# Performance work log

Hardware: AMD Instinct MI355X
Metric: run time of the kernel (lower is better)

Reference implementation:

```python
import jax, jax.numpy as jnp
import numpy as np
import math

D_MODEL = 1024
N_HEADS = 16
B, L, K = 2, 512, 4


def sinusoidal_pe(n, dim):
    # matches SinusoidalEmbedding buffer pe[:n]
    position = jnp.arange(n, dtype=jnp.float32)[:, None]
    div_term = jnp.exp(jnp.arange(0, dim, 2, dtype=jnp.float32) * (-math.log(10000.0) / dim))
    ang = position * div_term  # [n, dim//2]
    pe = jnp.zeros((n, dim), dtype=jnp.float32)
    pe = pe.at[:, 0::2].set(jnp.sin(ang))
    pe = pe.at[:, 1::2].set(jnp.cos(ang))
    return pe


def setup_inputs() -> dict:
    key = jax.random.key(0)
    ks = jax.random.split(key, 8)
    s = 1.0 / math.sqrt(D_MODEL)
    return {
        "h": jax.random.normal(ks[0], (B, L, K, D_MODEL), dtype=jnp.float32),
        "probs": jax.random.uniform(ks[1], (B, L, K), dtype=jnp.float32),
        "Wq": jax.random.normal(ks[2], (D_MODEL, D_MODEL), dtype=jnp.float32) * s,
        "bq": jnp.zeros((D_MODEL,), dtype=jnp.float32),
        "Wk": jax.random.normal(ks[3], (D_MODEL, D_MODEL), dtype=jnp.float32) * s,
        "bk": jnp.zeros((D_MODEL,), dtype=jnp.float32),
        "Wv": jax.random.normal(ks[4], (D_MODEL, D_MODEL), dtype=jnp.float32) * s,
        "bv": jnp.zeros((D_MODEL,), dtype=jnp.float32),
        "Wo": jax.random.normal(ks[5], (D_MODEL, D_MODEL), dtype=jnp.float32) * s,
        "bo": jnp.zeros((D_MODEL,), dtype=jnp.float32),
        "prob_bias_scale": jnp.float32(1.0),
        "n_heads": N_HEADS,
    }


def reference(h, probs, Wq, bq, Wk, bk, Wv, bv, Wo, bo, prob_bias_scale, n_heads):
    Bh, Lh, kh, D = h.shape
    N = Lh * kh
    hd = D // n_heads
    scale = hd ** (-0.5)

    h_flat = h.reshape(Bh, N, D) + sinusoidal_pe(N, D)[None]  # [B, N, D]
    probs_flat = probs.reshape(Bh, N)

    # torch Linear: x @ W.T + b
    q = (h_flat @ Wq.T + bq).reshape(Bh, N, n_heads, hd).transpose(0, 2, 1, 3)
    key = (h_flat @ Wk.T + bk).reshape(Bh, N, n_heads, hd).transpose(0, 2, 1, 3)
    v = (h_flat @ Wv.T + bv).reshape(Bh, N, n_heads, hd).transpose(0, 2, 1, 3)

    scores = jnp.einsum("bhnd,bhmd->bhnm", q, key) * scale  # [B,H,N,N]
    prob_bias = jnp.log(probs_flat + 1e-8)[:, None, None, :]  # bias on key axis
    scores = scores + prob_bias_scale * prob_bias
    attn = jax.nn.softmax(scores, axis=-1)  # dropout is identity in eval
    out = jnp.einsum("bhnm,bhmd->bhnd", attn, v)
    out = out.transpose(0, 2, 1, 3).reshape(Bh, N, D)
    out = out @ Wo.T + bo
    return out.reshape(Bh, Lh, kh, D)
```

## Files before the change

kernel.cpp:

```cpp
#include <hip/hip_runtime.h>

typedef _Float16 h8 __attribute__((ext_vector_type(8)));
typedef _Float16 h4 __attribute__((ext_vector_type(4)));
typedef float f32x4 __attribute__((ext_vector_type(4)));

#define NSEQ 2048
#define DMODEL 1024
#define HD 64
#define C2 0.1803368801111244f

#define OFF_HPE  (size_t)0
#define OFF_WQ   (size_t)8388608
#define OFF_WK   (size_t)10485760
#define OFF_WV   (size_t)12582912
#define OFF_WO   (size_t)14680064
#define OFF_Q    (size_t)16777216
#define OFF_K    (size_t)25165824
#define OFF_VT   (size_t)33554432
#define OFF_AO   (size_t)41943040
#define OFF_PB   (size_t)50331648

#define GLL(g, l) __builtin_amdgcn_global_load_lds( \
    (const __attribute__((address_space(1))) unsigned int*)(const void*)(g), \
    (__attribute__((address_space(3))) unsigned int*)(l), 16, 0, 0)

#if __has_builtin(__builtin_amdgcn_mfma_f32_16x16x16f16)
#define HAVE_MFMA16 1
#else
#define HAVE_MFMA16 0
#endif

__global__ void hpe_kernel(const float* __restrict__ h, _Float16* __restrict__ hpe) {
    int idx = blockIdx.x * blockDim.x + threadIdx.x;
    int row = idx >> 9;
    int i2  = idx & 511;
    int n = row & (NSEQ - 1);
    const float kTerm = -9.210340371976184f / 1024.0f;
    float div = expf((float)(2 * i2) * kTerm);
    float ang = (float)n * div;
    float s = sinf(ang), c = cosf(ang);
    int base = row * DMODEL + 2 * i2;
    hpe[base]     = (_Float16)(h[base] + s);
    hpe[base + 1] = (_Float16)(h[base + 1] + c);
}

__global__ void cast4_kernel(const float* __restrict__ w0, const float* __restrict__ w1,
                             const float* __restrict__ w2, const float* __restrict__ w3,
                             _Float16* __restrict__ d0, _Float16* __restrict__ d1,
                             _Float16* __restrict__ d2, _Float16* __restrict__ d3) {
    int i = blockIdx.x * blockDim.x + threadIdx.x;
    int which = i >> 18, idx = i & 262143;
    const float* s = which == 0 ? w0 : which == 1 ? w1 : which == 2 ? w2 : w3;
    _Float16* d    = which == 0 ? d0 : which == 1 ? d1 : which == 2 ? d2 : d3;
    float4 v = ((const float4*)s)[idx];
    union { _Float16 hh[4]; uint2 u; } o;
    o.hh[0] = (_Float16)v.x; o.hh[1] = (_Float16)v.y;
    o.hh[2] = (_Float16)v.z; o.hh[3] = (_Float16)v.w;
    ((uint2*)d)[idx] = o.u;
}

__global__ void pb_kernel(const float* __restrict__ probs, const float* __restrict__ pbs,
                          float* __restrict__ pb) {
    int i = blockIdx.x * blockDim.x + threadIdx.x;
    pb[i] = pbs[0] * log2f(probs[i] + 1e-8f);
}

__global__ __launch_bounds__(256) void gemm_qkv(
    const _Float16* __restrict__ A,
    const _Float16* __restrict__ Wqp, const _Float16* __restrict__ Wkp, const _Float16* __restrict__ Wvp,
    const float* __restrict__ bqp, const float* __restrict__ bkp, const float* __restrict__ bvp,
    _Float16* __restrict__ qb, _Float16* __restrict__ kb, _Float16* __restrict__ vt)
{
    __shared__ __align__(16) _Float16 As[128][64];
    __shared__ __align__(16) _Float16 Bs[128][64];
    int widx = blockIdx.y >> 3;
    const _Float16* W = widx == 0 ? Wqp : widx == 1 ? Wkp : Wvp;
    const float* bias = widx == 0 ? bqp : widx == 1 ? bkp : bvp;
    int tm = blockIdx.x * 128;
    int tn = (blockIdx.y & 7) * 128;
    int t = threadIdx.x;
    int wave = t >> 6, lane = t & 63;
    int wr = (wave >> 1) * 64, wc = (wave & 1) * 64;
    int lr = lane & 15, lg = lane >> 4;

    f32x4 acc[4][4] = {};

    int grow = lane >> 3;
    int gcol = (lane & 7) * 8;
    const _Float16* Aptr = A + (size_t)(tm + wave * 8 + grow) * DMODEL + gcol;
    const _Float16* Wptr = W + (size_t)(tn + wave * 8 + grow) * DMODEL + gcol;

    for (int k0 = 0; k0 < DMODEL; k0 += 64) {
        __syncthreads();
        #pragma unroll
        for (int i = 0; i < 4; ++i)
            GLL(Aptr + (size_t)i * 32 * DMODEL + k0, &As[i * 32 + wave * 8][0]);
        #pragma unroll
        for (int i = 0; i < 4; ++i)
            GLL(Wptr + (size_t)i * 32 * DMODEL + k0, &Bs[i * 32 + wave * 8][0]);
        __syncthreads();
        #pragma unroll
        for (int kk = 0; kk < 2; ++kk) {
            h8 af[4], bf[4];
            #pragma unroll
            for (int mi = 0; mi < 4; ++mi) af[mi] = *(const h8*)&As[wr + mi * 16 + lr][kk * 32 + lg * 8];
            #pragma unroll
            for (int ni = 0; ni < 4; ++ni) bf[ni] = *(const h8*)&Bs[wc + ni * 16 + lr][kk * 32 + lg * 8];
            #pragma unroll
            for (int mi = 0; mi < 4; ++mi)
                #pragma unroll
                for (int ni = 0; ni < 4; ++ni)
                    acc[mi][ni] = __builtin_amdgcn_mfma_f32_16x16x32_f16(af[mi], bf[ni], acc[mi][ni], 0, 0, 0);
        }
    }

    #pragma unroll
    for (int mi = 0; mi < 4; ++mi)
        #pragma unroll
        for (int ni = 0; ni < 4; ++ni) {
            int col = tn + wc + ni * 16 + lr;
            float bv = bias[col];
            if (widx < 2) {
                _Float16* dst = widx == 0 ? qb : kb;
                #pragma unroll
                for (int j = 0; j < 4; ++j) {
                    int row = tm + wr + mi * 16 + lg * 4 + j;
                    dst[(size_t)row * DMODEL + col] = (_Float16)(acc[mi][ni][j] + bv);
                }
            } else {
                int row0 = tm + wr + mi * 16 + lg * 4;
                int b = row0 >> 11, n0 = row0 & 2047;
                h4 pk;
                #pragma unroll
                for (int j = 0; j < 4; ++j) pk[j] = (_Float16)(acc[mi][ni][j] + bv);
                *(h4*)&vt[((size_t)b * 1024 + col) * 2048 + n0] = pk;
            }
        }
}

__global__ __launch_bounds__(256) void gemm_ao(
    const _Float16* __restrict__ A, const _Float16* __restrict__ W,
    const float* __restrict__ bias, float* __restrict__ C)
{
    __shared__ __align__(16) _Float16 As[64][64];
    __shared__ __align__(16) _Float16 Bs[128][64];
    int tm = blockIdx.x * 64;
    int tn = blockIdx.y * 128;
    int t = threadIdx.x;
    int wave = t >> 6, lane = t & 63;
    int wr = (wave >> 1) * 32, wc = (wave & 1) * 64;
    int lr = lane & 15, lg = lane >> 4;

    f32x4 acc[2][4] = {};

    int grow = lane >> 3;
    int gcol = (lane & 7) * 8;
    const _Float16* Aptr = A + (size_t)(tm + wave * 8 + grow) * DMODEL + gcol;
    const _Float16* Wptr = W + (size_t)(tn + wave * 8 + grow) * DMODEL + gcol;

    for (int k0 = 0; k0 < DMODEL; k0 += 64) {
        __syncthreads();
        #pragma unroll
        for (int i = 0; i < 2; ++i)
            GLL(Aptr + (size_t)i * 32 * DMODEL + k0, &As[i * 32 + wave * 8][0]);
        #pragma unroll
        for (int i = 0; i < 4; ++i)
            GLL(Wptr + (size_t)i * 32 * DMODEL + k0, &Bs[i * 32 + wave * 8][0]);
        __syncthreads();
        #pragma unroll
        for (int kk = 0; kk < 2; ++kk) {
            h8 af[2], bf[4];
            #pragma unroll
            for (int mi = 0; mi < 2; ++mi) af[mi] = *(const h8*)&As[wr + mi * 16 + lr][kk * 32 + lg * 8];
            #pragma unroll
            for (int ni = 0; ni < 4; ++ni) bf[ni] = *(const h8*)&Bs[wc + ni * 16 + lr][kk * 32 + lg * 8];
            #pragma unroll
            for (int mi = 0; mi < 2; ++mi)
                #pragma unroll
                for (int ni = 0; ni < 4; ++ni)
                    acc[mi][ni] = __builtin_amdgcn_mfma_f32_16x16x32_f16(af[mi], bf[ni], acc[mi][ni], 0, 0, 0);
        }
    }

    #pragma unroll
    for (int mi = 0; mi < 2; ++mi)
        #pragma unroll
        for (int ni = 0; ni < 4; ++ni)
            #pragma unroll
            for (int j = 0; j < 4; ++j) {
                int row = tm + wr + mi * 16 + lg * 4 + j;
                int col = tn + wc + ni * 16 + lr;
                C[(size_t)row * DMODEL + col] = acc[mi][ni][j] + bias[col];
            }
}

#define QT 64
#define KT 64

#define SWZ(row, bytecol) ((row) * 128 + ((bytecol) ^ (((row) & 7) << 4)))

__global__ __launch_bounds__(256, 4) void flash_kernel(
    const _Float16* __restrict__ Qb,
    const _Float16* __restrict__ Kb,
    const _Float16* __restrict__ Vt,
    const float* __restrict__ pb,
    _Float16* __restrict__ AO)
{
    __shared__ __align__(16) char KsB[64 * 128];
    __shared__ __align__(16) char VsB[64 * 128];
#if !HAVE_MFMA16
    __shared__ __align__(16) _Float16 Ps[4][16][72];
#endif
    int bh = blockIdx.y;
    int b = bh >> 4, h = bh & 15;
    int q0 = blockIdx.x * QT;
    int t = threadIdx.x, wave = t >> 6, lane = t & 63;
    int lr = lane & 15, lg = lane >> 4;

    const _Float16* Khead  = Kb + (size_t)b * NSEQ * DMODEL + h * HD;
    const _Float16* Vthead = Vt + ((size_t)b * 1024 + h * HD) * NSEQ;
    const float* pbb = pb + b * NSEQ;

    const _Float16* Qrow = Qb + ((size_t)b * NSEQ + q0 + wave * 16 + lr) * DMODEL + h * HD;
    h8 qf0 = *(const h8*)&Qrow[lg * 8];
    h8 qf1 = *(const h8*)&Qrow[32 + lg * 8];

    float mrun = -INFINITY, lrun = 0.f;
    f32x4 oacc[4] = {};

    int srow = t >> 2;
    int sc = (t & 3) * 32;

    for (int k0 = 0; k0 < NSEQ; k0 += KT) {
        f32x4 pbv[4];
        #pragma unroll
        for (int ci = 0; ci < 4; ++ci)
            pbv[ci] = *(const f32x4*)&pbb[k0 + ci * 16 + lg * 4];

        __syncthreads();
        *(h8*)(KsB + SWZ(srow, sc))      = *(const h8*)&Khead[(size_t)(k0 + srow) * DMODEL + (sc >> 1)];
        *(h8*)(KsB + SWZ(srow, sc + 16)) = *(const h8*)&Khead[(size_t)(k0 + srow) * DMODEL + (sc >> 1) + 8];
        *(h8*)(VsB + SWZ(srow, sc))      = *(const h8*)&Vthead[(size_t)srow * NSEQ + k0 + (sc >> 1)];
        *(h8*)(VsB + SWZ(srow, sc + 16)) = *(const h8*)&Vthead[(size_t)srow * NSEQ + k0 + (sc >> 1) + 8];
        __syncthreads();

        f32x4 s[4] = {};
        #pragma unroll
        for (int ci = 0; ci < 4; ++ci) {
            h8 kf = *(const h8*)(KsB + SWZ(ci * 16 + lr, lg * 16));
            s[ci] = __builtin_amdgcn_mfma_f32_16x16x32_f16(kf, qf0, s[ci], 0, 0, 0);
        }
        #pragma unroll
        for (int ci = 0; ci < 4; ++ci) {
            h8 kf = *(const h8*)(KsB + SWZ(ci * 16 + lr, 64 + lg * 16));
            s[ci] = __builtin_amdgcn_mfma_f32_16x16x32_f16(kf, qf1, s[ci], 0, 0, 0);
        }

        float p[4][4];
        float sm = -INFINITY;
        #pragma unroll
        for (int ci = 0; ci < 4; ++ci)
            #pragma unroll
            for (int j = 0; j < 4; ++j) {
                float vv = fmaf(s[ci][j], C2, pbv[ci][j]);
                p[ci][j] = vv;
                sm = fmaxf(sm, vv);
            }
        sm = fmaxf(sm, __shfl_xor(sm, 16));
        sm = fmaxf(sm, __shfl_xor(sm, 32));
        float newm = fmaxf(mrun, sm);
        float fs = __builtin_amdgcn_exp2f(mrun - newm);
        float rs = 0.f;
        #pragma unroll
        for (int ci = 0; ci < 4; ++ci)
            #pragma unroll
            for (int j = 0; j < 4; ++j) {
                float e = __builtin_amdgcn_exp2f(p[ci][j] - newm);
                p[ci][j] = e;
                rs += e;
            }
        rs += __shfl_xor(rs, 16);
        rs += __shfl_xor(rs, 32);
        lrun = lrun * fs + rs;
        mrun = newm;

        #pragma unroll
        for (int j = 0; j < 4; ++j) {
            float fsj = __shfl(fs, (lane & 48) | (lg * 4 + j), 64);
            #pragma unroll
            for (int ni = 0; ni < 4; ++ni) oacc[ni][j] *= fsj;
        }

#if HAVE_MFMA16
        #pragma unroll
        for (int ci = 0; ci < 4; ++ci) {
            h4 pa;
            #pragma unroll
            for (int j = 0; j < 4; ++j) pa[j] = (_Float16)p[ci][j];
            #pragma unroll
            for (int ni = 0; ni < 4; ++ni) {
                h4 vf = *(const h4*)(VsB + SWZ(ni * 16 + lr, ci * 32 + lg * 8));
                oacc[ni] = __builtin_amdgcn_mfma_f32_16x16x16f16(pa, vf, oacc[ni], 0, 0, 0);
            }
        }
#else
        #pragma unroll
        for (int ci = 0; ci < 4; ++ci) {
            union { _Float16 hh[4]; uint2 u; } pk;
            #pragma unroll
            for (int j = 0; j < 4; ++j) pk.hh[j] = (_Float16)p[ci][j];
            *(uint2*)&Ps[wave][lr][ci * 16 + lg * 4] = pk.u;
        }
        asm volatile("s_waitcnt lgkmcnt(0)" ::: "memory");
        __builtin_amdgcn_sched_barrier(0);
        #pragma unroll
        for (int kb2 = 0; kb2 < 2; ++kb2) {
            h8 pa = *(const h8*)&Ps[wave][lr][kb2 * 32 + lg * 8];
            #pragma unroll
            for (int ni = 0; ni < 4; ++ni) {
                h8 vf = *(const h8*)(VsB + SWZ(ni * 16 + lr, kb2 * 64 + lg * 16));
                oacc[ni] = __builtin_amdgcn_mfma_f32_16x16x32_f16(pa, vf, oacc[ni], 0, 0, 0);
            }
        }
#endif
    }

    #pragma unroll
    for (int j = 0; j < 4; ++j) {
        float lj = __shfl(lrun, (lane & 48) | (lg * 4 + j), 64);
        float inv = 1.0f / lj;
        int row = q0 + wave * 16 + lg * 4 + j;
        #pragma unroll
        for (int ni = 0; ni < 4; ++ni)
            AO[((size_t)b * NSEQ + row) * DMODEL + h * HD + ni * 16 + lr] = (_Float16)(oacc[ni][j] * inv);
    }
}

extern "C" void kernel_launch(void* const* d_in, const int* in_sizes, int n_in,
                              void* d_out, int out_size, void* d_ws, size_t ws_size,
                              hipStream_t stream) {
    const float* h    = (const float*)d_in[0];
    const float* prob = (const float*)d_in[1];
    const float* Wq   = (const float*)d_in[2];
    const float* bq   = (const float*)d_in[3];
    const float* Wk   = (const float*)d_in[4];
    const float* bk   = (const float*)d_in[5];
    const float* Wv   = (const float*)d_in[6];
    const float* bv   = (const float*)d_in[7];
    const float* Wo   = (const float*)d_in[8];
    const float* bo   = (const float*)d_in[9];
    const float* pbs  = (const float*)d_in[10];

    char* ws = (char*)d_ws;
    _Float16* hpe  = (_Float16*)(ws + OFF_HPE);
    _Float16* wq16 = (_Float16*)(ws + OFF_WQ);
    _Float16* wk16 = (_Float16*)(ws + OFF_WK);
    _Float16* wv16 = (_Float16*)(ws + OFF_WV);
    _Float16* wo16 = (_Float16*)(ws + OFF_WO);
    _Float16* qb   = (_Float16*)(ws + OFF_Q);
    _Float16* kb16 = (_Float16*)(ws + OFF_K);
    _Float16* vt   = (_Float16*)(ws + OFF_VT);
    _Float16* ao   = (_Float16*)(ws + OFF_AO);
    float*    pbuf = (float*)(ws + OFF_PB);

    hpe_kernel<<<dim3(8192), dim3(256), 0, stream>>>(h, hpe);
    cast4_kernel<<<dim3(4096), dim3(256), 0, stream>>>(Wq, Wk, Wv, Wo, wq16, wk16, wv16, wo16);
    pb_kernel<<<dim3(16), dim3(256), 0, stream>>>(prob, pbs, pbuf);

    gemm_qkv<<<dim3(32, 24), dim3(256), 0, stream>>>(hpe, wq16, wk16, wv16, bq, bk, bv, qb, kb16, vt);

    flash_kernel<<<dim3(32, 32), dim3(256), 0, stream>>>(qb, kb16, vt, pbuf, ao);

    gemm_ao<<<dim3(64, 8), dim3(256), 0, stream>>>(ao, wo16, bo, (float*)d_out);
}
```

Measured before the change: 247.1 us.

## Fold softmax scale into Wq, lazy rescale, MFMA row sums, vectorize PE kernel

The softmax scale (log2e/sqrt(hd)) is folded into the Q weight cast and bias, so scores come straight out of the QK MFMA with the log-prob bias preloaded as the accumulator. The online softmax now rescales only when some row max increases (wave-wide vote), computes row sums with an extra MFMA against a ones vector, and always uses the LDS P path with V fragments loaded early. The positional-encoding kernel is vectorized to 8 elements per thread using hardware exp2/sin/cos on fractional revolutions. These changes cut per-tile VALU and shuffle work in attention and memory traffic in the prologue. In exchange there are extra MFMAs and some precision risk from the rtz packing and hardware trig.

```diff
diff --git a/kernel.cpp b/kernel.cpp
--- a/kernel.cpp
+++ b/kernel.cpp
@@ -2,6 +2,7 @@
 
 typedef _Float16 h8 __attribute__((ext_vector_type(8)));
 typedef _Float16 h4 __attribute__((ext_vector_type(4)));
+typedef __fp16 fp16x2 __attribute__((ext_vector_type(2)));
 typedef float f32x4 __attribute__((ext_vector_type(4)));
 
 #define NSEQ 2048
@@ -24,24 +25,29 @@
     (const __attribute__((address_space(1))) unsigned int*)(const void*)(g), \
     (__attribute__((address_space(3))) unsigned int*)(l), 16, 0, 0)
 
-#if __has_builtin(__builtin_amdgcn_mfma_f32_16x16x16f16)
-#define HAVE_MFMA16 1
-#else
-#define HAVE_MFMA16 0
-#endif
-
 __global__ void hpe_kernel(const float* __restrict__ h, _Float16* __restrict__ hpe) {
     int idx = blockIdx.x * blockDim.x + threadIdx.x;
-    int row = idx >> 9;
-    int i2  = idx & 511;
+    int row = idx >> 7;
+    int c8 = (idx & 127) * 8;
     int n = row & (NSEQ - 1);
-    const float kTerm = -9.210340371976184f / 1024.0f;
-    float div = expf((float)(2 * i2) * kTerm);
-    float ang = (float)n * div;
-    float s = sinf(ang), c = cosf(ang);
-    int base = row * DMODEL + 2 * i2;
-    hpe[base]     = (_Float16)(h[base] + s);
-    hpe[base + 1] = (_Float16)(h[base + 1] + c);
+    const float kL = -0.025952563241307517f;
+    const float kInv2Pi = 0.15915494309189535f;
+    union { float4 f4[2]; float f[8]; } in;
+    in.f4[0] = *(const float4*)&h[(size_t)row * DMODEL + c8];
+    in.f4[1] = *(const float4*)&h[(size_t)row * DMODEL + c8 + 4];
+    union { _Float16 hh[8]; uint4 u; } out;
+    #pragma unroll
+    for (int p = 0; p < 4; ++p) {
+        int i2 = (c8 >> 1) + p;
+        float div = __builtin_amdgcn_exp2f((float)i2 * kL);
+        float rev = (float)n * div * kInv2Pi;
+        float rf = __builtin_amdgcn_fractf(rev);
+        float s = __builtin_amdgcn_sinf(rf);
+        float c = __builtin_amdgcn_cosf(rf);
+        out.hh[2 * p]     = (_Float16)(in.f[2 * p] + s);
+        out.hh[2 * p + 1] = (_Float16)(in.f[2 * p + 1] + c);
+    }
+    *(uint4*)&hpe[(size_t)row * DMODEL + c8] = out.u;
 }
 
 __global__ void cast4_kernel(const float* __restrict__ w0, const float* __restrict__ w1,
@@ -52,10 +58,11 @@
     int which = i >> 18, idx = i & 262143;
     const float* s = which == 0 ? w0 : which == 1 ? w1 : which == 2 ? w2 : w3;
     _Float16* d    = which == 0 ? d0 : which == 1 ? d1 : which == 2 ? d2 : d3;
+    float sc = which == 0 ? C2 : 1.0f;
     float4 v = ((const float4*)s)[idx];
     union { _Float16 hh[4]; uint2 u; } o;
-    o.hh[0] = (_Float16)v.x; o.hh[1] = (_Float16)v.y;
-    o.hh[2] = (_Float16)v.z; o.hh[3] = (_Float16)v.w;
+    o.hh[0] = (_Float16)(v.x * sc); o.hh[1] = (_Float16)(v.y * sc);
+    o.hh[2] = (_Float16)(v.z * sc); o.hh[3] = (_Float16)(v.w * sc);
     ((uint2*)d)[idx] = o.u;
 }
 
@@ -76,6 +83,7 @@
     int widx = blockIdx.y >> 3;
     const _Float16* W = widx == 0 ? Wqp : widx == 1 ? Wkp : Wvp;
     const float* bias = widx == 0 ? bqp : widx == 1 ? bkp : bvp;
+    float bscale = widx == 0 ? C2 : 1.0f;
     int tm = blockIdx.x * 128;
     int tn = (blockIdx.y & 7) * 128;
     int t = threadIdx.x;
@@ -119,7 +127,7 @@
         #pragma unroll
         for (int ni = 0; ni < 4; ++ni) {
             int col = tn + wc + ni * 16 + lr;
-            float bv = bias[col];
+            float bv = bias[col] * bscale;
             if (widx < 2) {
                 _Float16* dst = widx == 0 ? qb : kb;
                 #pragma unroll
@@ -208,9 +216,7 @@
 {
     __shared__ __align__(16) char KsB[64 * 128];
     __shared__ __align__(16) char VsB[64 * 128];
-#if !HAVE_MFMA16
     __shared__ __align__(16) _Float16 Ps[4][16][72];
-#endif
     int bh = blockIdx.y;
     int b = bh >> 4, h = bh & 15;
     int q0 = blockIdx.x * QT;
@@ -225,17 +231,21 @@
     h8 qf0 = *(const h8*)&Qrow[lg * 8];
     h8 qf1 = *(const h8*)&Qrow[32 + lg * 8];
 
-    float mrun = -INFINITY, lrun = 0.f;
+    const h8 vones = { (_Float16)1, (_Float16)1, (_Float16)1, (_Float16)1,
+                       (_Float16)1, (_Float16)1, (_Float16)1, (_Float16)1 };
+
+    float mrun = -INFINITY;
     f32x4 oacc[4] = {};
+    f32x4 lsum = {};
 
     int srow = t >> 2;
     int sc = (t & 3) * 32;
 
     for (int k0 = 0; k0 < NSEQ; k0 += KT) {
-        f32x4 pbv[4];
+        f32x4 s[4];
         #pragma unroll
         for (int ci = 0; ci < 4; ++ci)
-            pbv[ci] = *(const f32x4*)&pbb[k0 + ci * 16 + lg * 4];
+            s[ci] = *(const f32x4*)&pbb[k0 + ci * 16 + lg * 4];
 
         __syncthreads();
         *(h8*)(KsB + SWZ(srow, sc))      = *(const h8*)&Khead[(size_t)(k0 + srow) * DMODEL + (sc >> 1)];
@@ -244,7 +254,6 @@
         *(h8*)(VsB + SWZ(srow, sc + 16)) = *(const h8*)&Vthead[(size_t)srow * NSEQ + k0 + (sc >> 1) + 8];
         __syncthreads();
 
-        f32x4 s[4] = {};
         #pragma unroll
         for (int ci = 0; ci < 4; ++ci) {
             h8 kf = *(const h8*)(KsB + SWZ(ci * 16 + lr, lg * 16));
@@ -256,79 +265,62 @@
             s[ci] = __builtin_amdgcn_mfma_f32_16x16x32_f16(kf, qf1, s[ci], 0, 0, 0);
         }
 
-        float p[4][4];
-        float sm = -INFINITY;
+        float sm = s[0][0];
         #pragma unroll
         for (int ci = 0; ci < 4; ++ci)
             #pragma unroll
-            for (int j = 0; j < 4; ++j) {
-                float vv = fmaf(s[ci][j], C2, pbv[ci][j]);
-                p[ci][j] = vv;
-                sm = fmaxf(sm, vv);
-            }
+            for (int j = 0; j < 4; ++j) sm = fmaxf(sm, s[ci][j]);
         sm = fmaxf(sm, __shfl_xor(sm, 16));
         sm = fmaxf(sm, __shfl_xor(sm, 32));
-        float newm = fmaxf(mrun, sm);
-        float fs = __builtin_amdgcn_exp2f(mrun - newm);
-        float rs = 0.f;
-        #pragma unroll
-        for (int ci = 0; ci < 4; ++ci)
+
+        bool need = __any(sm > mrun);
+        float newm = need ? fmaxf(mrun, sm) : mrun;
+
+        #pragma unroll
+        for (int ci = 0; ci < 4; ++ci) {
+            fp16x2 a = __builtin_amdgcn_cvt_pkrtz(__builtin_amdgcn_exp2f(s[ci][0] - newm),
+                                                  __builtin_amdgcn_exp2f(s[ci][1] - newm));
+            fp16x2 b2 = __builtin_amdgcn_cvt_pkrtz(__builtin_amdgcn_exp2f(s[ci][2] - newm),
+                                                   __builtin_amdgcn_exp2f(s[ci][3] - newm));
+            union { fp16x2 hh[2]; uint2 u; } pk;
+            pk.hh[0] = a; pk.hh[1] = b2;
+            *(uint2*)&Ps[wave][lr][ci * 16 + lg * 4] = pk.u;
+        }
+
+        h8 vf[2][4];
+        #pragma unroll
+        for (int kb = 0; kb < 2; ++kb)
+            #pragma unroll
+            for (int ni = 0; ni < 4; ++ni)
+                vf[kb][ni] = *(const h8*)(VsB + SWZ(ni * 16 + lr, kb * 64 + lg * 16));
+
+        if (need) {
+            float fs = __builtin_amdgcn_exp2f(mrun - newm);
+            mrun = newm;
             #pragma unroll
             for (int j = 0; j < 4; ++j) {
-                float e = __builtin_amdgcn_exp2f(p[ci][j] - newm);
-                p[ci][j] = e;
-                rs += e;
+                float fsj = __shfl(fs, (lane & 48) | (lg * 4 + j), 64);
+                #pragma unroll
+                for (int ni = 0; ni < 4; ++ni) oacc[ni][j] *= fsj;
+                lsum[j] *= fsj;
             }
-        rs += __shfl_xor(rs, 16);
-        rs += __shfl_xor(rs, 32);
-        lrun = lrun * fs + rs;
-        mrun = newm;
-
-        #pragma unroll
-        for (int j = 0; j < 4; ++j) {
-            float fsj = __shfl(fs, (lane & 48) | (lg * 4 + j), 64);
-            #pragma unroll
-            for (int ni = 0; ni < 4; ++ni) oacc[ni][j] *= fsj;
-        }
-
-#if HAVE_MFMA16
-        #pragma unroll
-        for (int ci = 0; ci < 4; ++ci) {
-            h4 pa;
-            #pragma unroll
-            for (int j = 0; j < 4; ++j) pa[j] = (_Float16)p[ci][j];
-            #pragma unroll
-            for (int ni = 0; ni < 4; ++ni) {
-                h4 vf = *(const h4*)(VsB + SWZ(ni * 16 + lr, ci * 32 + lg * 8));
-                oacc[ni] = __builtin_amdgcn_mfma_f32_16x16x16f16(pa, vf, oacc[ni], 0, 0, 0);
-            }
-        }
-#else
-        #pragma unroll
-        for (int ci = 0; ci < 4; ++ci) {
-            union { _Float16 hh[4]; uint2 u; } pk;
-            #pragma unroll
-            for (int j = 0; j < 4; ++j) pk.hh[j] = (_Float16)p[ci][j];
-            *(uint2*)&Ps[wave][lr][ci * 16 + lg * 4] = pk.u;
-        }
+        }
+
         asm volatile("s_waitcnt lgkmcnt(0)" ::: "memory");
-        __builtin_amdgcn_sched_barrier(0);
-        #pragma unroll
-        for (int kb2 = 0; kb2 < 2; ++kb2) {
-            h8 pa = *(const h8*)&Ps[wave][lr][kb2 * 32 + lg * 8];
-            #pragma unroll
-            for (int ni = 0; ni < 4; ++ni) {
-                h8 vf = *(const h8*)(VsB + SWZ(ni * 16 + lr, kb2 * 64 + lg * 16));
-                oacc[ni] = __builtin_amdgcn_mfma_f32_16x16x32_f16(pa, vf, oacc[ni], 0, 0, 0);
-            }
-        }
-#endif
+
+        #pragma unroll
+        for (int kb = 0; kb < 2; ++kb) {
+            h8 pa = *(const h8*)&Ps[wave][lr][kb * 32 + lg * 8];
+            #pragma unroll
+            for (int ni = 0; ni < 4; ++ni)
+                oacc[ni] = __builtin_amdgcn_mfma_f32_16x16x32_f16(pa, vf[kb][ni], oacc[ni], 0, 0, 0);
+            lsum = __builtin_amdgcn_mfma_f32_16x16x32_f16(pa, vones, lsum, 0, 0, 0);
+        }
     }
 
     #pragma unroll
     for (int j = 0; j < 4; ++j) {
-        float lj = __shfl(lrun, (lane & 48) | (lg * 4 + j), 64);
-        float inv = 1.0f / lj;
+        float inv = 1.0f / lsum[j];
         int row = q0 + wave * 16 + lg * 4 + j;
         #pragma unroll
         for (int ni = 0; ni < 4; ++ni)
@@ -363,7 +355,7 @@
     _Float16* ao   = (_Float16*)(ws + OFF_AO);
     float*    pbuf = (float*)(ws + OFF_PB);
 
-    hpe_kernel<<<dim3(8192), dim3(256), 0, stream>>>(h, hpe);
+    hpe_kernel<<<dim3(2048), dim3(256), 0, stream>>>(h, hpe);
     cast4_kernel<<<dim3(4096), dim3(256), 0, stream>>>(Wq, Wk, Wv, Wo, wq16, wk16, wv16, wo16);
     pb_kernel<<<dim3(16), dim3(256), 0, stream>>>(prob, pbs, pbuf);
 
```

Result: no change. 246.1 us (-0.4%).
